# Kernel tuning notes

Hardware: AMD Instinct MI355X
Metric: run time of the kernel (lower is better)

Reference implementation:

```python
import jax, jax.numpy as jnp
import numpy as np

B, S, D, H = 4, 2048, 1024, 16
DQKV = max(1, D // H)  # 64


def setup_inputs() -> dict:
    key = jax.random.key(0)
    ks = jax.random.split(key, 12)
    std = 1.0 / np.sqrt(D)
    inp = {
        "query": jax.random.normal(ks[0], (B, S, D), dtype=jnp.float32),
        "key": jax.random.normal(ks[1], (B, S, D), dtype=jnp.float32),
        "value": jax.random.normal(ks[2], (B, S, D), dtype=jnp.float32),
        # per-head projection weights, stacked over heads: [H, DQKV, D] (torch Linear layout [out,in])
        "wq": jax.random.uniform(ks[3], (H, DQKV, D), jnp.float32, -std, std),
        "bq": jax.random.uniform(ks[4], (H, DQKV), jnp.float32, -std, std),
        "wk": jax.random.uniform(ks[5], (H, DQKV, D), jnp.float32, -std, std),
        "bk": jax.random.uniform(ks[6], (H, DQKV), jnp.float32, -std, std),
        "wv": jax.random.uniform(ks[7], (H, DQKV, D), jnp.float32, -std, std),
        "bv": jax.random.uniform(ks[8], (H, DQKV), jnp.float32, -std, std),
        # output projection: [D, H*DQKV]
        "wo": jax.random.uniform(ks[9], (D, H * DQKV), jnp.float32, -1.0 / np.sqrt(H * DQKV), 1.0 / np.sqrt(H * DQKV)),
        "bo": jax.random.uniform(ks[10], (D,), jnp.float32, -1.0 / np.sqrt(H * DQKV), 1.0 / np.sqrt(H * DQKV)),
    }
    return inp


def reference(query, key, value, wq, bq, wk, bk, wv, bv, wo, bo):
    # Per-head linear projections (batched over heads): [B, H, S, DQKV]
    Q = jnp.einsum("bsd,hed->bhse", query, wq) + bq[None, :, None, :]
    K = jnp.einsum("bsd,hed->bhse", key, wk) + bk[None, :, None, :]
    V = jnp.einsum("bsd,hed->bhse", value, wv) + bv[None, :, None, :]
    scale = jnp.asarray(DQKV, Q.dtype) ** 0.5
    # Full N x N attention scores per head (matches naive bmm+softmax+bmm)
    scores = jnp.einsum("bhse,bhte->bhst", Q, K) / scale
    attn = jax.nn.softmax(scores, axis=-1)
    ctx = jnp.einsum("bhst,bhte->bhse", attn, V)  # [B, H, S, DQKV]
    # Concat over heads in head-major order: [B, S, H*DQKV]
    concat = jnp.transpose(ctx, (0, 2, 1, 3)).reshape(ctx.shape[0], ctx.shape[2], H * DQKV)
    return jnp.einsum("bsf,df->bsd", concat, wo) + bo
```

## Files before the change

kernel.cpp:

```cpp
#include <hip/hip_runtime.h>
#include <stdint.h>
#include <stddef.h>


typedef __attribute__((ext_vector_type(8))) short short8;
typedef __attribute__((ext_vector_type(4))) float f32x4;

#if __has_builtin(__builtin_amdgcn_exp2f)
#define EXP2F __builtin_amdgcn_exp2f
#else
#define EXP2F exp2f
#endif
#if __has_builtin(__builtin_amdgcn_rcpf)
#define RCPF __builtin_amdgcn_rcpf
#else
#define RCPF(x) (1.0f / (x))
#endif

__device__ __forceinline__ uint16_t f2bf(float f) {
  uint32_t u = __builtin_bit_cast(uint32_t, f);
  u += 0x7FFFu + ((u >> 16) & 1u);
  return (uint16_t)(u >> 16);
}

__device__ __forceinline__ void gld16(const void* g, void* l) {
  __builtin_amdgcn_global_load_lds((const __attribute__((address_space(1))) void*)g,
                                   (__attribute__((address_space(3))) void*)l, 16, 0, 0);
}

__global__ __launch_bounds__(256) void cast3(const float* __restrict__ s0, const float* __restrict__ s1,
                                             const float* __restrict__ s2, uint16_t* __restrict__ d0,
                                             uint16_t* __restrict__ d1, uint16_t* __restrict__ d2,
                                             int n4) {
  const int z = blockIdx.y;
  const float* s = z == 0 ? s0 : (z == 1 ? s1 : s2);
  uint16_t* d = z == 0 ? d0 : (z == 1 ? d1 : d2);
  int i = blockIdx.x * 256 + threadIdx.x;
  if (i >= n4) return;
  float4 v = ((const float4*)s)[i];
  ushort4 o;
  o.x = f2bf(v.x); o.y = f2bf(v.y); o.z = f2bf(v.z); o.w = f2bf(v.w);
  ((ushort4*)d)[i] = o;
}

__global__ __launch_bounds__(256) void cast4(const float* __restrict__ s0, const float* __restrict__ s1,
                                             const float* __restrict__ s2, const float* __restrict__ s3,
                                             uint16_t* __restrict__ d0, uint16_t* __restrict__ d1,
                                             uint16_t* __restrict__ d2, uint16_t* __restrict__ d3,
                                             int n4) {
  const int z = blockIdx.y;
  const float* s = z == 0 ? s0 : (z == 1 ? s1 : (z == 2 ? s2 : s3));
  uint16_t* d = z == 0 ? d0 : (z == 1 ? d1 : (z == 2 ? d2 : d3));
  int i = blockIdx.x * 256 + threadIdx.x;
  if (i >= n4) return;
  float4 v = ((const float4*)s)[i];
  ushort4 o;
  o.x = f2bf(v.x); o.y = f2bf(v.y); o.z = f2bf(v.z); o.w = f2bf(v.w);
  ((ushort4*)d)[i] = o;
}

__device__ __forceinline__ void gemm_core(const uint16_t* __restrict__ A,
                                          const uint16_t* __restrict__ Bw,
                                          uint16_t* As, uint16_t* Bs,
                                          f32x4 acc[4][4], int m0, int n0) {
  constexpr int K = 1024;
  const int tid = threadIdx.x;
  const int w = tid >> 6, l = tid & 63;
  const int ln = l & 15, quad = l >> 4;
  const int wm = (w >> 1) * 64, wn = (w & 1) * 64;

  const uint16_t* Ag[4];
  const uint16_t* Bg[4];
  int lofs[4];
#pragma unroll
  for (int c = 0; c < 4; ++c) {
    const int f = c * 256 + tid;
    const int row = f >> 3, cp = f & 7, g = (cp - row) & 7;
    Ag[c] = A + (size_t)(m0 + row) * K + g * 8;
    Bg[c] = Bw + (size_t)(n0 + row) * K + g * 8;
    lofs[c] = f * 8;
  }
  int colk[2];
#pragma unroll
  for (int kk = 0; kk < 2; ++kk) colk[kk] = (kk * 4 + quad + ln) & 7;

  for (int k0 = 0; k0 < K; k0 += 64) {
    __syncthreads();
#pragma unroll
    for (int c = 0; c < 4; ++c) {
      gld16(Ag[c] + k0, As + lofs[c]);
      gld16(Bg[c] + k0, Bs + lofs[c]);
    }
    __syncthreads();
#pragma unroll
    for (int kk = 0; kk < 2; ++kk) {
      short8 a[4], b[4];
#pragma unroll
      for (int mt = 0; mt < 4; ++mt)
        a[mt] = *(const short8*)(As + (wm + mt * 16 + ln) * 64 + colk[kk] * 8);
#pragma unroll
      for (int nt = 0; nt < 4; ++nt)
        b[nt] = *(const short8*)(Bs + (wn + nt * 16 + ln) * 64 + colk[kk] * 8);
#pragma unroll
      for (int mt = 0; mt < 4; ++mt)
#pragma unroll
        for (int nt = 0; nt < 4; ++nt)
          acc[mt][nt] = __builtin_amdgcn_mfma_f32_16x16x32_bf16(a[mt], b[nt], acc[mt][nt], 0, 0, 0);
    }
  }
}

__global__ __launch_bounds__(256) void gemm_qkv(const uint16_t* __restrict__ Xq, const uint16_t* __restrict__ Xk,
                                                const uint16_t* __restrict__ Xv, const uint16_t* __restrict__ Wq,
                                                const uint16_t* __restrict__ Wk, const uint16_t* __restrict__ Wv,
                                                const float* __restrict__ bq, const float* __restrict__ bk,
                                                const float* __restrict__ bv, uint16_t* __restrict__ Qb,
                                                uint16_t* __restrict__ Kb, uint16_t* __restrict__ Vtb,
                                                float qscale, int zbase) {
  __shared__ __attribute__((aligned(16))) uint16_t As[128 * 64];
  __shared__ __attribute__((aligned(16))) uint16_t Bs[128 * 64];
  const int lin = blockIdx.x + (blockIdx.y << 3) + (blockIdx.z << 9);
  const int per = gridDim.z << 3;
  const int xcd = lin & 7, local = lin >> 3;
  const int mz = xcd * per + (local >> 3);
  const int z = (mz >> 6) + zbase;
  const int m0 = (mz & 63) * 128, n0 = (local & 7) * 128;

  const uint16_t* A = z == 0 ? Xq : (z == 1 ? Xk : Xv);
  const uint16_t* Bw = z == 0 ? Wq : (z == 1 ? Wk : Wv);
  const float* bias = z == 0 ? bq : (z == 1 ? bk : bv);
  uint16_t* Cout = z == 0 ? Qb : (z == 1 ? Kb : Vtb);
  const float scale = z == 0 ? qscale : 1.0f;

  f32x4 acc[4][4] = {};
  gemm_core(A, Bw, As, Bs, acc, m0, n0);

  const int tid = threadIdx.x;
  const int w = tid >> 6, l = tid & 63;
  const int ln = l & 15, quad = l >> 4;
  const int wm = (w >> 1) * 64, wn = (w & 1) * 64;
#pragma unroll
  for (int nt = 0; nt < 4; ++nt) {
    const int col = n0 + wn + nt * 16 + ln;
    const float bv_ = bias[col];
    const int h = col >> 6, e = col & 63;
#pragma unroll
    for (int mt = 0; mt < 4; ++mt) {
#pragma unroll
      for (int i = 0; i < 4; ++i) {
        const int row = m0 + wm + mt * 16 + quad * 4 + i;
        const int b_ = row >> 11, s = row & 2047;
        const float v = (acc[mt][nt][i] + bv_) * scale;
        if (z != 2) {
          Cout[(size_t)(b_ * 16 + h) * 131072 + s * 64 + e] = f2bf(v);
        } else {
          Cout[(size_t)(b_ * 16 + h) * 131072 + e * 2048 + s] = f2bf(v);
        }
      }
    }
  }
}

__global__ __launch_bounds__(256) void gemm_out(const uint16_t* __restrict__ A, const uint16_t* __restrict__ Bw,
                                                const float* __restrict__ bias, float* __restrict__ Cout) {
  __shared__ __attribute__((aligned(16))) uint16_t As[128 * 64];
  __shared__ __attribute__((aligned(16))) uint16_t Bs[128 * 64];
  const int lin = blockIdx.x + (blockIdx.y << 3);
  const int xcd = lin & 7, local = lin >> 3;
  const int m0 = (xcd * 8 + (local >> 3)) * 128, n0 = (local & 7) * 128;
  f32x4 acc[4][4] = {};
  gemm_core(A, Bw, As, Bs, acc, m0, n0);

  const int tid = threadIdx.x;
  const int w = tid >> 6, l = tid & 63;
  const int ln = l & 15, quad = l >> 4;
  const int wm = (w >> 1) * 64, wn = (w & 1) * 64;
#pragma unroll
  for (int nt = 0; nt < 4; ++nt) {
    const int col = n0 + wn + nt * 16 + ln;
    const float bv_ = bias[col];
#pragma unroll
    for (int mt = 0; mt < 4; ++mt)
#pragma unroll
      for (int i = 0; i < 4; ++i) {
        const int row = m0 + wm + mt * 16 + quad * 4 + i;
        Cout[(size_t)row * 1024 + col] = acc[mt][nt][i] + bv_;
      }
  }
}

__global__ __launch_bounds__(256, 4) void attn(const uint16_t* __restrict__ Qb,
                                               const uint16_t* __restrict__ Kb,
                                               const uint16_t* __restrict__ Vtb,
                                               uint16_t* __restrict__ Ctx) {
  __shared__ __attribute__((aligned(16))) uint16_t Ks[64 * 64];
  __shared__ __attribute__((aligned(16))) uint16_t Vs[64 * 64];
  __shared__ __attribute__((aligned(16))) uint16_t Ps[4 * 2 * 16 * 72];
  const int tid = threadIdx.x;
  const int w = tid >> 6, l = tid & 63;
  const int ln = l & 15, quad = l >> 4;
  const int lin = blockIdx.x + (blockIdx.y << 4);
  const int slot = lin >> 3;
  const int bh = (lin & 7) * 8 + (slot >> 4);
  const int q0 = (slot & 15) * 128;
  const int b = bh >> 4, h = bh & 15;
  const uint16_t* Qh = Qb + (size_t)bh * 131072;
  const uint16_t* Kh = Kb + (size_t)bh * 131072;
  const uint16_t* Vth = Vtb + (size_t)bh * 131072;

  short8 qf[2][2];
#pragma unroll
  for (int sub = 0; sub < 2; ++sub)
#pragma unroll
    for (int ks = 0; ks < 2; ++ks)
      qf[sub][ks] = *(const short8*)(Qh + (size_t)(q0 + w * 32 + sub * 16 + ln) * 64 + ks * 32 + quad * 8);

  short8 ones;
#pragma unroll
  for (int j = 0; j < 8; ++j) ones[j] = (short)0x3F80;

  int col[2];
#pragma unroll
  for (int ks = 0; ks < 2; ++ks) col[ks] = (ks * 4 + quad + ln) & 7;
  uint16_t* Pw = Ps + w * 2304;

  f32x4 oacc[2][4] = {};
  f32x4 lacc[2] = {};

  for (int t0 = 0; t0 < 2048; t0 += 64) {
    __syncthreads();
#pragma unroll
    for (int c = 0; c < 2; ++c) {
      const int f = w * 128 + c * 64 + l;
      const int t = f >> 3, g = ((f & 7) - t) & 7;
      gld16(Kh + (size_t)(t0 + t) * 64 + g * 8, Ks + (w * 128 + c * 64) * 8);
      gld16(Vth + (size_t)t * 2048 + t0 + g * 8, Vs + (w * 128 + c * 64) * 8);
    }
    __syncthreads();

    f32x4 sacc[2][4] = {};
    __builtin_amdgcn_s_setprio(1);
#pragma unroll
    for (int nt = 0; nt < 4; ++nt) {
      const int t = nt * 16 + ln;
#pragma unroll
      for (int ks = 0; ks < 2; ++ks) {
        const short8 kf = *(const short8*)(Ks + (t * 8 + col[ks]) * 8);
        sacc[0][nt] = __builtin_amdgcn_mfma_f32_16x16x32_bf16(kf, qf[0][ks], sacc[0][nt], 0, 0, 0);
        sacc[1][nt] = __builtin_amdgcn_mfma_f32_16x16x32_bf16(kf, qf[1][ks], sacc[1][nt], 0, 0, 0);
      }
    }
    __builtin_amdgcn_s_setprio(0);

#pragma unroll
    for (int sub = 0; sub < 2; ++sub)
#pragma unroll
      for (int nt = 0; nt < 4; ++nt) {
        const uint32_t u0 = __builtin_bit_cast(uint32_t, EXP2F(sacc[sub][nt][0]));
        const uint32_t u1 = __builtin_bit_cast(uint32_t, EXP2F(sacc[sub][nt][1]));
        const uint32_t u2 = __builtin_bit_cast(uint32_t, EXP2F(sacc[sub][nt][2]));
        const uint32_t u3 = __builtin_bit_cast(uint32_t, EXP2F(sacc[sub][nt][3]));
        uint2 dd;
        dd.x = ((u0 + 0x7FFFu + ((u0 >> 16) & 1u)) >> 16) |
               ((u1 + 0x7FFFu + ((u1 >> 16) & 1u)) & 0xFFFF0000u);
        dd.y = ((u2 + 0x7FFFu + ((u2 >> 16) & 1u)) >> 16) |
               ((u3 + 0x7FFFu + ((u3 >> 16) & 1u)) & 0xFFFF0000u);
        *(uint2*)(Pw + sub * 1152 + ln * 72 + nt * 16 + quad * 4) = dd;
      }

#pragma unroll
    for (int ks = 0; ks < 2; ++ks) {
      const short8 pf0 = *(const short8*)(Pw + ln * 72 + ks * 32 + quad * 8);
      const short8 pf1 = *(const short8*)(Pw + 1152 + ln * 72 + ks * 32 + quad * 8);
      __builtin_amdgcn_s_setprio(1);
      lacc[0] = __builtin_amdgcn_mfma_f32_16x16x32_bf16(pf0, ones, lacc[0], 0, 0, 0);
      lacc[1] = __builtin_amdgcn_mfma_f32_16x16x32_bf16(pf1, ones, lacc[1], 0, 0, 0);
#pragma unroll
      for (int nt = 0; nt < 4; ++nt) {
        const int e = nt * 16 + ln;
        const short8 vf = *(const short8*)(Vs + (e * 8 + col[ks]) * 8);
        oacc[0][nt] = __builtin_amdgcn_mfma_f32_16x16x32_bf16(pf0, vf, oacc[0][nt], 0, 0, 0);
        oacc[1][nt] = __builtin_amdgcn_mfma_f32_16x16x32_bf16(pf1, vf, oacc[1][nt], 0, 0, 0);
      }
      __builtin_amdgcn_s_setprio(0);
    }
  }

#pragma unroll
  for (int sub = 0; sub < 2; ++sub) {
    float inv[4];
#pragma unroll
    for (int i = 0; i < 4; ++i) inv[i] = RCPF(lacc[sub][i]);
#pragma unroll
    for (int nt = 0; nt < 4; ++nt)
#pragma unroll
      for (int i = 0; i < 4; ++i) {
        const float v = oacc[sub][nt][i] * inv[i];
        const int s = q0 + w * 32 + sub * 16 + quad * 4 + i;
        Ctx[(size_t)(b * 2048 + s) * 1024 + h * 64 + nt * 16 + ln] = f2bf(v);
      }
  }
}

extern "C" void kernel_launch(void* const* d_in, const int* in_sizes, int n_in,
                              void* d_out, int out_size, void* d_ws, size_t ws_size,
                              hipStream_t stream) {
  const float* q = (const float*)d_in[0];
  const float* k = (const float*)d_in[1];
  const float* v = (const float*)d_in[2];
  const float* wq = (const float*)d_in[3];
  const float* bq = (const float*)d_in[4];
  const float* wk = (const float*)d_in[5];
  const float* bk = (const float*)d_in[6];
  const float* wv = (const float*)d_in[7];
  const float* bv = (const float*)d_in[8];
  const float* wo = (const float*)d_in[9];
  const float* bo = (const float*)d_in[10];
  float* out = (float*)d_out;

  uint16_t* ws = (uint16_t*)d_ws;
  uint16_t* Xq = ws;
  uint16_t* Xk = Xq + 8388608;
  uint16_t* Xv = Xk + 8388608;
  uint16_t* Wq = Xv + 8388608;
  uint16_t* Wk = Wq + 1048576;
  uint16_t* Wv = Wk + 1048576;
  uint16_t* Wo = Wv + 1048576;
  uint16_t* Qb = Wo + 1048576;
  uint16_t* Kb = Qb + 8388608;
  uint16_t* Ctx = Xq;

  const size_t fused_elems = 46137344u + 8388608u;
  const bool fused = ws_size >= fused_elems * sizeof(uint16_t);
  uint16_t* Vtb = fused ? (Kb + 8388608) : Xk;

  cast3<<<dim3(8192, 3), 256, 0, stream>>>(q, k, v, Xq, Xk, Xv, 2097152);
  cast4<<<dim3(1024, 4), 256, 0, stream>>>(wq, wk, wv, wo, Wq, Wk, Wv, Wo, 262144);

  const float qscale = 0.125f * 1.4426950408889634f;
  if (fused) {
    gemm_qkv<<<dim3(8, 64, 3), 256, 0, stream>>>(Xq, Xk, Xv, Wq, Wk, Wv, bq, bk, bv,
                                                 Qb, Kb, Vtb, qscale, 0);
  } else {
    gemm_qkv<<<dim3(8, 64, 1), 256, 0, stream>>>(Xq, Xk, Xv, Wq, Wk, Wv, bq, bk, bv,
                                                 Qb, Kb, Vtb, qscale, 0);
    gemm_qkv<<<dim3(8, 64, 1), 256, 0, stream>>>(Xq, Xk, Xv, Wq, Wk, Wv, bq, bk, bv,
                                                 Qb, Kb, Vtb, qscale, 1);
    gemm_qkv<<<dim3(8, 64, 1), 256, 0, stream>>>(Xq, Xk, Xv, Wq, Wk, Wv, bq, bk, bv,
                                                 Qb, Kb, Vtb, qscale, 2);
  }

  attn<<<dim3(16, 64), 256, 0, stream>>>(Qb, Kb, Vtb, Ctx);

  gemm_out<<<dim3(8, 64), 256, 0, stream>>>(Ctx, Wo, bo, out);
}
```

Before: 367.5 us.

## Double-buffer LDS tiles in the projection GEMMs to overlap loads with MFMA

The shared GEMM core now uses two LDS buffer pairs. It issues the global-to-LDS loads for the next 64-wide K slice before computing on the current slice, which removes one barrier per iteration and hides load latency behind the MFMA work. The trade-off is that LDS per block doubles to 64KB, which can reduce the number of resident blocks per CU. The fully unrolled 16-step loop also grows code size. The change applies to both the QKV and output projection GEMMs.

```diff
diff --git a/kernel.cpp b/kernel.cpp
--- a/kernel.cpp
+++ b/kernel.cpp
@@ -59,9 +59,39 @@
   ((ushort4*)d)[i] = o;
 }
 
+__device__ __forceinline__ void gemm_stage(const uint16_t* const* Ag, const uint16_t* const* Bg,
+                                           const int* lofs, uint16_t* As, uint16_t* Bs, int k0) {
+#pragma unroll
+  for (int c = 0; c < 4; ++c) {
+    gld16(Ag[c] + k0, As + lofs[c]);
+    gld16(Bg[c] + k0, Bs + lofs[c]);
+  }
+}
+
+__device__ __forceinline__ void gemm_compute(const uint16_t* As, const uint16_t* Bs,
+                                             f32x4 acc[4][4], int wm, int wn, int ln, int quad,
+                                             const int* colk) {
+#pragma unroll
+  for (int kk = 0; kk < 2; ++kk) {
+    short8 a[4], b[4];
+#pragma unroll
+    for (int mt = 0; mt < 4; ++mt)
+      a[mt] = *(const short8*)(As + (wm + mt * 16 + ln) * 64 + colk[kk] * 8);
+#pragma unroll
+    for (int nt = 0; nt < 4; ++nt)
+      b[nt] = *(const short8*)(Bs + (wn + nt * 16 + ln) * 64 + colk[kk] * 8);
+#pragma unroll
+    for (int mt = 0; mt < 4; ++mt)
+#pragma unroll
+      for (int nt = 0; nt < 4; ++nt)
+        acc[mt][nt] = __builtin_amdgcn_mfma_f32_16x16x32_bf16(a[mt], b[nt], acc[mt][nt], 0, 0, 0);
+  }
+}
+
 __device__ __forceinline__ void gemm_core(const uint16_t* __restrict__ A,
                                           const uint16_t* __restrict__ Bw,
-                                          uint16_t* As, uint16_t* Bs,
+                                          uint16_t* As0, uint16_t* Bs0,
+                                          uint16_t* As1, uint16_t* Bs1,
                                           f32x4 acc[4][4], int m0, int n0) {
   constexpr int K = 1024;
   const int tid = threadIdx.x;
@@ -84,29 +114,17 @@
 #pragma unroll
   for (int kk = 0; kk < 2; ++kk) colk[kk] = (kk * 4 + quad + ln) & 7;
 
-  for (int k0 = 0; k0 < K; k0 += 64) {
-    __syncthreads();
-#pragma unroll
-    for (int c = 0; c < 4; ++c) {
-      gld16(Ag[c] + k0, As + lofs[c]);
-      gld16(Bg[c] + k0, Bs + lofs[c]);
-    }
-    __syncthreads();
-#pragma unroll
-    for (int kk = 0; kk < 2; ++kk) {
-      short8 a[4], b[4];
-#pragma unroll
-      for (int mt = 0; mt < 4; ++mt)
-        a[mt] = *(const short8*)(As + (wm + mt * 16 + ln) * 64 + colk[kk] * 8);
-#pragma unroll
-      for (int nt = 0; nt < 4; ++nt)
-        b[nt] = *(const short8*)(Bs + (wn + nt * 16 + ln) * 64 + colk[kk] * 8);
-#pragma unroll
-      for (int mt = 0; mt < 4; ++mt)
-#pragma unroll
-        for (int nt = 0; nt < 4; ++nt)
-          acc[mt][nt] = __builtin_amdgcn_mfma_f32_16x16x32_bf16(a[mt], b[nt], acc[mt][nt], 0, 0, 0);
-    }
+  gemm_stage(Ag, Bg, lofs, As0, Bs0, 0);
+  __syncthreads();
+#pragma unroll
+  for (int s = 0; s < 16; ++s) {
+    uint16_t* Asn = (s & 1) ? As0 : As1;
+    uint16_t* Bsn = (s & 1) ? Bs0 : Bs1;
+    const uint16_t* Asc = (s & 1) ? As1 : As0;
+    const uint16_t* Bsc = (s & 1) ? Bs1 : Bs0;
+    if (s < 15) gemm_stage(Ag, Bg, lofs, Asn, Bsn, (s + 1) * 64);
+    gemm_compute(Asc, Bsc, acc, wm, wn, ln, quad, colk);
+    if (s < 15) __syncthreads();
   }
 }
 
@@ -117,8 +135,10 @@
                                                 const float* __restrict__ bv, uint16_t* __restrict__ Qb,
                                                 uint16_t* __restrict__ Kb, uint16_t* __restrict__ Vtb,
                                                 float qscale, int zbase) {
-  __shared__ __attribute__((aligned(16))) uint16_t As[128 * 64];
-  __shared__ __attribute__((aligned(16))) uint16_t Bs[128 * 64];
+  __shared__ __attribute__((aligned(16))) uint16_t As0[128 * 64];
+  __shared__ __attribute__((aligned(16))) uint16_t Bs0[128 * 64];
+  __shared__ __attribute__((aligned(16))) uint16_t As1[128 * 64];
+  __shared__ __attribute__((aligned(16))) uint16_t Bs1[128 * 64];
   const int lin = blockIdx.x + (blockIdx.y << 3) + (blockIdx.z << 9);
   const int per = gridDim.z << 3;
   const int xcd = lin & 7, local = lin >> 3;
@@ -133,7 +153,7 @@
   const float scale = z == 0 ? qscale : 1.0f;
 
   f32x4 acc[4][4] = {};
-  gemm_core(A, Bw, As, Bs, acc, m0, n0);
+  gemm_core(A, Bw, As0, Bs0, As1, Bs1, acc, m0, n0);
 
   const int tid = threadIdx.x;
   const int w = tid >> 6, l = tid & 63;
@@ -163,13 +183,15 @@
 
 __global__ __launch_bounds__(256) void gemm_out(const uint16_t* __restrict__ A, const uint16_t* __restrict__ Bw,
                                                 const float* __restrict__ bias, float* __restrict__ Cout) {
-  __shared__ __attribute__((aligned(16))) uint16_t As[128 * 64];
-  __shared__ __attribute__((aligned(16))) uint16_t Bs[128 * 64];
+  __shared__ __attribute__((aligned(16))) uint16_t As0[128 * 64];
+  __shared__ __attribute__((aligned(16))) uint16_t Bs0[128 * 64];
+  __shared__ __attribute__((aligned(16))) uint16_t As1[128 * 64];
+  __shared__ __attribute__((aligned(16))) uint16_t Bs1[128 * 64];
   const int lin = blockIdx.x + (blockIdx.y << 3);
   const int xcd = lin & 7, local = lin >> 3;
   const int m0 = (xcd * 8 + (local >> 3)) * 128, n0 = (local & 7) * 128;
   f32x4 acc[4][4] = {};
-  gemm_core(A, Bw, As, Bs, acc, m0, n0);
+  gemm_core(A, Bw, As0, Bs0, As1, Bs1, acc, m0, n0);
 
   const int tid = threadIdx.x;
   const int w = tid >> 6, l = tid & 63;
```

After: 370.9 us. Within noise of the previous version (+0.9%).
